# Optimization experiments

Hardware: AMD Instinct MI355X
Metric: run time of the kernel (lower is better)

## Reference

```python
import jax, jax.numpy as jnp
import numpy as np

KH, KW = 3, 3
SH, SW = 1, 1
DH, DW = 1, 1
OFFSET_GROUPS = 1
WEIGHT_GROUPS = 1


def setup_inputs() -> dict:
    key = jax.random.key(0)
    k1, k2, k3, k4 = jax.random.split(key, 4)
    B, C, H, W = 8, 128, 64, 64
    F = 128
    x = jax.random.normal(k1, (B, C, H, W), dtype=jnp.float32)
    offset = jax.random.normal(k2, (B, OFFSET_GROUPS * 2 * KH * KW, H, W), dtype=jnp.float32)
    mask = jax.random.uniform(k3, (B, OFFSET_GROUPS * KH * KW, H, W), dtype=jnp.float32)
    weight = jax.random.normal(k4, (F, C // WEIGHT_GROUPS, KH, KW), dtype=jnp.float32) * 0.05
    return {"x": x, "offset": offset, "mask": mask, "weight": weight}


def _deform_conv2d(x, offset, mask, weight):
    B, C, H, W = x.shape
    F = weight.shape[0]
    Ho, Wo = offset.shape[2], offset.shape[3]
    KK = KH * KW
    og = OFFSET_GROUPS
    Cg = C // og

    # SAME padding (TF convention, symmetric-ish: extra pad at bottom/right)
    pad_h = max((Ho - 1) * SH + (KH - 1) * DH + 1 - H, 0)
    pad_w = max((Wo - 1) * SW + (KW - 1) * DW + 1 - W, 0)
    pad_t, pad_l = pad_h // 2, pad_w // 2

    # offsets laid out as [B, og, KK, (dy,dx), Ho, Wo]
    off = offset.reshape(B, og, KK, 2, Ho, Wo)
    dy, dx = off[:, :, :, 0], off[:, :, :, 1]  # [B, og, KK, Ho, Wo]

    ki, kj = jnp.meshgrid(jnp.arange(KH), jnp.arange(KW), indexing="ij")
    ki = ki.reshape(KK)
    kj = kj.reshape(KK)
    base_y = (jnp.arange(Ho) * SH - pad_t)[None, :] + (ki * DH)[:, None]  # [KK, Ho]
    base_x = (jnp.arange(Wo) * SW - pad_l)[None, :] + (kj * DW)[:, None]  # [KK, Wo]

    py = base_y[None, None, :, :, None].astype(x.dtype) + dy  # [B, og, KK, Ho, Wo]
    px = base_x[None, None, :, None, :].astype(x.dtype) + dx

    y0 = jnp.floor(py)
    x0 = jnp.floor(px)
    ly = py - y0  # fractional parts
    lx = px - x0
    hy = 1.0 - ly
    hx = 1.0 - lx
    y0i = y0.astype(jnp.int32)
    x0i = x0.astype(jnp.int32)

    xg = x.reshape(B, og, Cg, H * W)

    def gather_corner(yi, xi):
        valid = (yi >= 0) & (yi < H) & (xi >= 0) & (xi < W)  # [B, og, KK, Ho, Wo]
        yc = jnp.clip(yi, 0, H - 1)
        xc = jnp.clip(xi, 0, W - 1)
        flat = (yc * W + xc).reshape(B, og, 1, KK * Ho * Wo)
        vals = jnp.take_along_axis(xg, flat, axis=3).reshape(B, og, Cg, KK, Ho, Wo)
        return vals * valid[:, :, None].astype(x.dtype)

    v00 = gather_corner(y0i, x0i)
    v01 = gather_corner(y0i, x0i + 1)
    v10 = gather_corner(y0i + 1, x0i)
    v11 = gather_corner(y0i + 1, x0i + 1)

    w00 = (hy * hx)[:, :, None]
    w01 = (hy * lx)[:, :, None]
    w10 = (ly * hx)[:, :, None]
    w11 = (ly * lx)[:, :, None]
    sampled = v00 * w00 + v01 * w01 + v10 * w10 + v11 * w11  # [B, og, Cg, KK, Ho, Wo]

    # modulation mask: [B, og, KK, Ho, Wo]
    m = mask.reshape(B, og, KK, Ho, Wo)
    sampled = sampled * m[:, :, None]

    # grouped matmul (weight_groups=1 -> plain); columns ordered c*KK + kk, matching
    # weight [F, C, KH, KW] flattened.
    cols = sampled.reshape(B, C * KK, Ho, Wo)
    out = jnp.einsum("fk,bkhw->bfhw", weight.reshape(F, C // WEIGHT_GROUPS * KK), cols)
    return out


def reference(x, offset, mask, weight):
    return _deform_conv2d(x, offset, mask, weight)
```

## Files before the change

kernel.cpp:

```cpp
#include <hip/hip_runtime.h>
#include <hip/hip_bf16.h>

typedef __attribute__((ext_vector_type(8))) short bf16x8;
typedef __attribute__((ext_vector_type(4))) float f32x4;
typedef __attribute__((ext_vector_type(2))) float f32x2;
typedef unsigned int uint32;
typedef unsigned short ushort_t;
typedef __attribute__((ext_vector_type(4))) uint32 u32x4;

__device__ __forceinline__ ushort_t f2bf(float f) {
    unsigned int u = __float_as_uint(f);
    u = (u + 0x7FFFu + ((u >> 16) & 1u)) >> 16;
    return (ushort_t)u;
}

__device__ __forceinline__ uint32 cvt_pk_bf16(float lo, float hi) {
    uint32 r;
    asm("v_cvt_pk_bf16_f32 %0, %1, %2" : "=v"(r) : "v"(lo), "v"(hi));
    return r;
}

__device__ __forceinline__ void gload_lds16(const void* g, void* l) {
    __builtin_amdgcn_global_load_lds(
        (const __attribute__((address_space(1))) uint32*)g,
        (__attribute__((address_space(3))) uint32*)l, 16, 0, 0);
}

__global__ __launch_bounds__(256) void prep_all(const float* __restrict__ x,
                                                const float* __restrict__ w,
                                                ushort_t* __restrict__ xt,
                                                ushort_t* __restrict__ wT2) {
    int bi = blockIdx.x;
    int t = threadIdx.x;
    if (bi >= 4096) {
        int idx = (bi - 4096) * 256 + t;
        int j  = idx & 7;
        int f  = (idx >> 3) & 127;
        int lu = (idx >> 10) & 3;
        int ks = (idx >> 12) & 3;
        int tap = idx >> 14;
        int c = ks * 32 + lu * 8 + j;
        wT2[idx] = f2bf(w[((size_t)f * 128 + c) * 9 + tap]);
        return;
    }
    __shared__ float tile[32][33];
    int b = bi & 7;
    int r2 = bi >> 3;
    int wb = r2 & 1, cb = (r2 >> 1) & 3, y = r2 >> 3;
    int lw = t & 31, lc = t >> 5;
    #pragma unroll
    for (int pass = 0; pass < 4; ++pass) {
        int c = cb * 32 + lc + pass * 8;
        tile[lc + pass * 8][lw] = x[(((size_t)b * 128 + c) * 64 + y) * 64 + wb * 32 + lw];
    }
    __syncthreads();
    int cc = t & 31, xl = t >> 5;
    #pragma unroll
    for (int pass = 0; pass < 4; ++pass) {
        int xll = xl + pass * 8;
        int xx = wb * 32 + xll;
        int c = cb * 32 + cc;
        int c2 = (((c >> 3) ^ (xx & 7)) << 3) | (c & 7);
        xt[(((size_t)b * 64 + y) * 64 + xx) * 128 + c2] = f2bf(tile[cc][xll]);
    }
}

__device__ __forceinline__ bf16x8 interp4(u32x4 c0, u32x4 c1, u32x4 c2, u32x4 c3,
                                          f32x4 wv) {
    uint32 rr[4];
    #pragma unroll
    for (int i = 0; i < 4; ++i) {
        f32x2 a, s;
        uint32 u = c0[i];
        a.x = __uint_as_float(u << 16); a.y = __uint_as_float(u & 0xffff0000u);
        s = a * wv.x;
        u = c1[i];
        a.x = __uint_as_float(u << 16); a.y = __uint_as_float(u & 0xffff0000u);
        s += a * wv.y;
        u = c2[i];
        a.x = __uint_as_float(u << 16); a.y = __uint_as_float(u & 0xffff0000u);
        s += a * wv.z;
        u = c3[i];
        a.x = __uint_as_float(u << 16); a.y = __uint_as_float(u & 0xffff0000u);
        s += a * wv.w;
        rr[i] = cvt_pk_bf16(s.x, s.y);
    }
    u32x4 q = {rr[0], rr[1], rr[2], rr[3]};
    return __builtin_bit_cast(bf16x8, q);
}

__global__ __launch_bounds__(1024, 4) void dcn_main(
    const float* __restrict__ offset, const float* __restrict__ mask,
    const ushort_t* __restrict__ xt, const ushort_t* __restrict__ wT2,
    float* __restrict__ out)
{
    __shared__ ushort_t xwin[7 * 64 * 128];
    __shared__ float  pws_l[9][64][4];
    __shared__ uint32 pos_l[9][64];

    int bi = blockIdx.x;
    int b = bi & 7, ho = bi >> 3;
    int t = threadIdx.x, lane = t & 63, wid = t >> 6;
    int pxg = wid & 3, ks = wid >> 2;
    int p = lane & 15, lu = lane >> 4;
    int px = pxg * 16 + p;
    int row0 = min(max(ho - 3, 0), 57);

    const char* xgb = (const char*)xt + (size_t)b * (64 * 64 * 256);

    {
        const char* ws = xgb + ((size_t)row0 << 14);
        #pragma unroll
        for (int r = 0; r < 7; ++r)
            gload_lds16(ws + (r * 1024 + t) * 16, (char*)xwin + (r * 1024 + t) * 16);
    }
    if (t < 576) {
        int k = t >> 6, pi = t & 63;
        int ki = k / 3, kj = k - ki * 3;
        float dy = offset[(((size_t)b * 18 + 2 * k)     * 64 + ho) * 64 + pi];
        float dx = offset[(((size_t)b * 18 + 2 * k + 1) * 64 + ho) * 64 + pi];
        float m  = mask  [(((size_t)b * 9  + k)         * 64 + ho) * 64 + pi];
        float py = (float)(ho - 1 + ki) + dy;
        float px_ = (float)(pi - 1 + kj) + dx;
        float y0f = floorf(py), x0f = floorf(px_);
        float ly = py - y0f, lx = px_ - x0f;
        float hy = 1.f - ly, hx = 1.f - lx;
        int y0 = (int)y0f, x0 = (int)x0f;
        int y1 = y0 + 1, x1 = x0 + 1;
        float vy0 = (y0 >= 0 && y0 < 64) ? 1.f : 0.f;
        float vy1 = (y1 >= 0 && y1 < 64) ? 1.f : 0.f;
        float vx0 = (x0 >= 0 && x0 < 64) ? 1.f : 0.f;
        float vx1 = (x1 >= 0 && x1 < 64) ? 1.f : 0.f;
        pws_l[k][pi][0] = hy * hx * m * vy0 * vx0;
        pws_l[k][pi][1] = hy * lx * m * vy0 * vx1;
        pws_l[k][pi][2] = ly * hx * m * vy1 * vx0;
        pws_l[k][pi][3] = ly * lx * m * vy1 * vx1;
        int y0c = min(max(y0, 0), 63), y1c = min(max(y1, 0), 63);
        int x0c = min(max(x0, 0), 63), x1c = min(max(x1, 0), 63);
        pos_l[k][pi] = (uint32)(y0c * 64 + x0c) | ((uint32)(y1c * 64 + x1c) << 16);
    }
    __syncthreads();

    f32x4 acc[8];
    #pragma unroll
    for (int i = 0; i < 8; ++i) acc[i] = (f32x4){0.f, 0.f, 0.f, 0.f};

    int klu = ks * 64 + lu * 16;

    #pragma unroll 1
    for (int tap = 0; tap < 9; ++tap) {
        uint32 pp = pos_l[tap][px];
        f32x4 wv = *(const f32x4*)pws_l[tap][px];
        int i00 = pp & 0xffffu, i11 = pp >> 16;
        int y0c = i00 >> 6, x0c = i00 & 63;
        int y1c = i11 >> 6, x1c = i11 & 63;
        u32x4 g[4];
        #pragma unroll
        for (int c = 0; c < 4; ++c) {
            int yc = (c < 2) ? y0c : y1c;
            int xc = (c & 1) ? x1c : x0c;
            int rl = yc - row0;
            int off = klu ^ ((xc & 7) << 4);
            bool inw = (unsigned)rl < 7u;
            const char* lp = (const char*)xwin + (((inw ? rl : 0) * 64 + xc) << 8) + off;
            g[c] = *(const u32x4*)lp;
            if (!inw) {
                const char* gp = xgb + (((size_t)yc * 64 + xc) << 8) + off;
                g[c] = *(const u32x4*)gp;
            }
        }
        bf16x8 bb = interp4(g[0], g[1], g[2], g[3], wv);

        const ushort_t* ab = wT2 + (size_t)(tap * 4 + ks) * 4096 + (lu * 128 + p) * 8;
        #pragma unroll
        for (int ft = 0; ft < 8; ++ft) {
            bf16x8 aa = *(const bf16x8*)(ab + ft * 128);
            acc[ft] = __builtin_amdgcn_mfma_f32_16x16x32_bf16(aa, bb, acc[ft], 0, 0, 0);
        }
    }

    __syncthreads();
    float* red = (float*)xwin;

    #define DUMP(SLOT)                                                          \
        do {                                                                    \
            _Pragma("unroll")                                                   \
            for (int ft = 0; ft < 8; ++ft)                                      \
                _Pragma("unroll")                                               \
                for (int r = 0; r < 4; ++r)                                     \
                    red[(SLOT) * 8192 + (ft * 16 + lu * 4 + r) * 64 + px] =     \
                        acc[ft][r];                                             \
        } while (0)
    #define ADDIN(SLOT)                                                         \
        do {                                                                    \
            _Pragma("unroll")                                                   \
            for (int ft = 0; ft < 8; ++ft)                                      \
                _Pragma("unroll")                                               \
                for (int r = 0; r < 4; ++r)                                     \
                    acc[ft][r] += red[(SLOT) * 8192                             \
                        + (ft * 16 + lu * 4 + r) * 64 + px];                    \
        } while (0)

    if (ks == 1) DUMP(0);
    if (ks == 3) DUMP(1);
    __syncthreads();
    if (ks == 0) ADDIN(0);
    if (ks == 2) ADDIN(1);
    __syncthreads();
    if (ks == 2) DUMP(0);
    __syncthreads();
    if (ks == 0) {
        ADDIN(0);
        float* outb = out + (size_t)b * 128 * 4096 + ho * 64;
        #pragma unroll
        for (int ft = 0; ft < 8; ++ft)
            #pragma unroll
            for (int r = 0; r < 4; ++r) {
                int f = ft * 16 + lu * 4 + r;
                outb[(size_t)f * 4096 + px] = acc[ft][r];
            }
    }
    #undef DUMP
    #undef ADDIN
}

extern "C" void kernel_launch(void* const* d_in, const int* in_sizes, int n_in,
                              void* d_out, int out_size, void* d_ws, size_t ws_size,
                              hipStream_t stream) {
    const float* x      = (const float*)d_in[0];
    const float* offset = (const float*)d_in[1];
    const float* mask   = (const float*)d_in[2];
    const float* weight = (const float*)d_in[3];
    float* out = (float*)d_out;

    ushort_t* xt  = (ushort_t*)d_ws;
    ushort_t* wT2 = xt + (size_t)8 * 64 * 64 * 128;
    if (ws_size < (size_t)(8 * 64 * 64 * 128 + 9 * 16384) * 2) return;

    prep_all<<<4672, 256, 0, stream>>>(x, weight, xt, wT2);
    dcn_main<<<512, 1024, 0, stream>>>(offset, mask, xt, wT2, out);
}
```

Before: 41.83 us.

## Process two output rows per block to reuse weights and the LDS window

Each block now computes two output rows (256 blocks instead of 512). It loads an 8-row input window into LDS and runs two MFMA pixel tiles per weight fragment, so every weight load feeds twice as many MFMAs. Bilinear weights are stored as bf16 and per-corner positions are precomputed with an in-window flag, which lets the LDS budget (about 155KB) hold the larger window. The costs are half as many blocks to fill the GPU, more accumulator registers, and slightly lower precision in the interpolation weights.

```diff
diff --git a/kernel.cpp b/kernel.cpp
--- a/kernel.cpp
+++ b/kernel.cpp
@@ -7,6 +7,7 @@
 typedef unsigned int uint32;
 typedef unsigned short ushort_t;
 typedef __attribute__((ext_vector_type(4))) uint32 u32x4;
+typedef __attribute__((ext_vector_type(2))) uint32 u32x2;
 
 __device__ __forceinline__ ushort_t f2bf(float f) {
     unsigned int u = __float_as_uint(f);
@@ -94,34 +95,37 @@
     const ushort_t* __restrict__ xt, const ushort_t* __restrict__ wT2,
     float* __restrict__ out)
 {
-    __shared__ ushort_t xwin[7 * 64 * 128];
-    __shared__ float  pws_l[9][64][4];
-    __shared__ uint32 pos_l[9][64];
+    __shared__ __align__(16) char smem[158720];
+    ushort_t* xwin = (ushort_t*)smem;
+    ushort_t* pwsl = (ushort_t*)(smem + 131072);
+    uint32*   posl = (uint32*)(smem + 140288);
 
     int bi = blockIdx.x;
-    int b = bi & 7, ho = bi >> 3;
+    int b = bi & 7, rp = bi >> 3;
+    int ho0 = rp * 2;
+    int row0 = min(max(ho0 - 3, 0), 56);
     int t = threadIdx.x, lane = t & 63, wid = t >> 6;
-    int pxg = wid & 3, ks = wid >> 2;
+    int ks = wid >> 2, rowg = (wid >> 1) & 1, pxg = wid & 1;
     int p = lane & 15, lu = lane >> 4;
-    int px = pxg * 16 + p;
-    int row0 = min(max(ho - 3, 0), 57);
+    int klu = (ks * 4 + lu) << 4;
 
     const char* xgb = (const char*)xt + (size_t)b * (64 * 64 * 256);
 
     {
         const char* ws = xgb + ((size_t)row0 << 14);
         #pragma unroll
-        for (int r = 0; r < 7; ++r)
+        for (int r = 0; r < 8; ++r)
             gload_lds16(ws + (r * 1024 + t) * 16, (char*)xwin + (r * 1024 + t) * 16);
     }
-    if (t < 576) {
-        int k = t >> 6, pi = t & 63;
+    for (int item = t; item < 1152; item += 1024) {
+        int k = item >> 7, pxx = item & 127;
+        int row = ho0 + (pxx >> 6), wo = pxx & 63;
         int ki = k / 3, kj = k - ki * 3;
-        float dy = offset[(((size_t)b * 18 + 2 * k)     * 64 + ho) * 64 + pi];
-        float dx = offset[(((size_t)b * 18 + 2 * k + 1) * 64 + ho) * 64 + pi];
-        float m  = mask  [(((size_t)b * 9  + k)         * 64 + ho) * 64 + pi];
-        float py = (float)(ho - 1 + ki) + dy;
-        float px_ = (float)(pi - 1 + kj) + dx;
+        float dy = offset[(((size_t)b * 18 + 2 * k)     * 64 + row) * 64 + wo];
+        float dx = offset[(((size_t)b * 18 + 2 * k + 1) * 64 + row) * 64 + wo];
+        float m  = mask  [(((size_t)b * 9  + k)         * 64 + row) * 64 + wo];
+        float py = (float)(row - 1 + ki) + dy;
+        float px_ = (float)(wo - 1 + kj) + dx;
         float y0f = floorf(py), x0f = floorf(px_);
         float ly = py - y0f, lx = px_ - x0f;
         float hy = 1.f - ly, hx = 1.f - lx;
@@ -131,74 +135,100 @@
         float vy1 = (y1 >= 0 && y1 < 64) ? 1.f : 0.f;
         float vx0 = (x0 >= 0 && x0 < 64) ? 1.f : 0.f;
         float vx1 = (x1 >= 0 && x1 < 64) ? 1.f : 0.f;
-        pws_l[k][pi][0] = hy * hx * m * vy0 * vx0;
-        pws_l[k][pi][1] = hy * lx * m * vy0 * vx1;
-        pws_l[k][pi][2] = ly * hx * m * vy1 * vx0;
-        pws_l[k][pi][3] = ly * lx * m * vy1 * vx1;
+        int base = (k * 128 + pxx) * 4;
+        pwsl[base + 0] = f2bf(hy * hx * m * vy0 * vx0);
+        pwsl[base + 1] = f2bf(hy * lx * m * vy0 * vx1);
+        pwsl[base + 2] = f2bf(ly * hx * m * vy1 * vx0);
+        pwsl[base + 3] = f2bf(ly * lx * m * vy1 * vx1);
         int y0c = min(max(y0, 0), 63), y1c = min(max(y1, 0), 63);
         int x0c = min(max(x0, 0), 63), x1c = min(max(x1, 0), 63);
-        pos_l[k][pi] = (uint32)(y0c * 64 + x0c) | ((uint32)(y1c * 64 + x1c) << 16);
-    }
-    __syncthreads();
-
-    f32x4 acc[8];
-    #pragma unroll
-    for (int i = 0; i < 8; ++i) acc[i] = (f32x4){0.f, 0.f, 0.f, 0.f};
-
-    int klu = ks * 64 + lu * 16;
-
-    #pragma unroll 1
-    for (int tap = 0; tap < 9; ++tap) {
-        uint32 pp = pos_l[tap][px];
-        f32x4 wv = *(const f32x4*)pws_l[tap][px];
-        int i00 = pp & 0xffffu, i11 = pp >> 16;
-        int y0c = i00 >> 6, x0c = i00 & 63;
-        int y1c = i11 >> 6, x1c = i11 & 63;
-        u32x4 g[4];
         #pragma unroll
         for (int c = 0; c < 4; ++c) {
             int yc = (c < 2) ? y0c : y1c;
             int xc = (c & 1) ? x1c : x0c;
-            int rl = yc - row0;
-            int off = klu ^ ((xc & 7) << 4);
-            bool inw = (unsigned)rl < 7u;
-            const char* lp = (const char*)xwin + (((inw ? rl : 0) * 64 + xc) << 8) + off;
-            g[c] = *(const u32x4*)lp;
-            if (!inw) {
-                const char* gp = xgb + (((size_t)yc * 64 + xc) << 8) + off;
-                g[c] = *(const u32x4*)gp;
+            uint32 inw = ((unsigned)(yc - row0) < 8u) ? 0x80u : 0u;
+            posl[base + c] = ((uint32)(yc * 64 + xc) << 8) | (uint32)(xc & 7) | inw;
+        }
+    }
+    __syncthreads();
+
+    f32x4 acc[8][2];
+    #pragma unroll
+    for (int i = 0; i < 8; ++i) {
+        acc[i][0] = (f32x4){0.f, 0.f, 0.f, 0.f};
+        acc[i][1] = (f32x4){0.f, 0.f, 0.f, 0.f};
+    }
+
+    int rbase = row0 << 14;
+
+    #pragma unroll 1
+    for (int tap = 0; tap < 9; ++tap) {
+        bf16x8 bfr[2];
+        #pragma unroll
+        for (int tile = 0; tile < 2; ++tile) {
+            int pxi = rowg * 64 + pxg * 32 + tile * 16 + p;
+            int pb = (tap * 128 + pxi) * 4;
+            u32x2 pw = *(const u32x2*)&pwsl[pb];
+            f32x4 wv;
+            wv.x = __uint_as_float(pw.x << 16);
+            wv.y = __uint_as_float(pw.x & 0xffff0000u);
+            wv.z = __uint_as_float(pw.y << 16);
+            wv.w = __uint_as_float(pw.y & 0xffff0000u);
+            u32x4 pv = *(const u32x4*)&posl[pb];
+            u32x4 g[4];
+            #pragma unroll
+            for (int c = 0; c < 4; ++c) {
+                uint32 v = pv[c];
+                int off = klu ^ (((int)v & 7) << 4);
+                int grec = (int)(v & 0xFFFFFF00u);
+                bool inw = (v & 0x80u) != 0;
+                const char* lp = (const char*)xwin + (inw ? (grec - rbase + off) : off);
+                g[c] = *(const u32x4*)lp;
+                if (!inw) {
+                    g[c] = *(const u32x4*)(xgb + grec + off);
+                }
+            }
+            bfr[tile] = interp4(g[0], g[1], g[2], g[3], wv);
+        }
+
+        const ushort_t* ab = wT2 + (size_t)(tap * 4 + ks) * 4096 + (lu * 128 + p) * 8;
+        #pragma unroll
+        for (int fq = 0; fq < 2; ++fq) {
+            #pragma unroll
+            for (int i = 0; i < 4; ++i) {
+                int ft = fq * 4 + i;
+                bf16x8 aa = *(const bf16x8*)(ab + ft * 128);
+                acc[ft][0] = __builtin_amdgcn_mfma_f32_16x16x32_bf16(aa, bfr[0], acc[ft][0], 0, 0, 0);
+                acc[ft][1] = __builtin_amdgcn_mfma_f32_16x16x32_bf16(aa, bfr[1], acc[ft][1], 0, 0, 0);
             }
         }
-        bf16x8 bb = interp4(g[0], g[1], g[2], g[3], wv);
-
-        const ushort_t* ab = wT2 + (size_t)(tap * 4 + ks) * 4096 + (lu * 128 + p) * 8;
-        #pragma unroll
-        for (int ft = 0; ft < 8; ++ft) {
-            bf16x8 aa = *(const bf16x8*)(ab + ft * 128);
-            acc[ft] = __builtin_amdgcn_mfma_f32_16x16x32_bf16(aa, bb, acc[ft], 0, 0, 0);
-        }
-    }
-
-    __syncthreads();
-    float* red = (float*)xwin;
-
-    #define DUMP(SLOT)                                                          \
-        do {                                                                    \
-            _Pragma("unroll")                                                   \
-            for (int ft = 0; ft < 8; ++ft)                                      \
-                _Pragma("unroll")                                               \
-                for (int r = 0; r < 4; ++r)                                     \
-                    red[(SLOT) * 8192 + (ft * 16 + lu * 4 + r) * 64 + px] =     \
-                        acc[ft][r];                                             \
+    }
+
+    __syncthreads();
+    float* red = (float*)smem;
+    int region = rowg * 2 + pxg;
+
+    #define DUMP(SLOT)                                                           \
+        do {                                                                     \
+            _Pragma("unroll")                                                    \
+            for (int ft = 0; ft < 8; ++ft)                                       \
+                _Pragma("unroll")                                                \
+                for (int tile = 0; tile < 2; ++tile)                             \
+                    _Pragma("unroll")                                            \
+                    for (int r = 0; r < 4; ++r)                                  \
+                        red[((((SLOT) * 4 + region) * 128 + ft * 16 + lu * 4 + r)\
+                             * 32) + tile * 16 + p] = acc[ft][tile][r];          \
         } while (0)
-    #define ADDIN(SLOT)                                                         \
-        do {                                                                    \
-            _Pragma("unroll")                                                   \
-            for (int ft = 0; ft < 8; ++ft)                                      \
-                _Pragma("unroll")                                               \
-                for (int r = 0; r < 4; ++r)                                     \
-                    acc[ft][r] += red[(SLOT) * 8192                             \
-                        + (ft * 16 + lu * 4 + r) * 64 + px];                    \
+    #define ADDIN(SLOT)                                                          \
+        do {                                                                     \
+            _Pragma("unroll")                                                    \
+            for (int ft = 0; ft < 8; ++ft)                                       \
+                _Pragma("unroll")                                                \
+                for (int tile = 0; tile < 2; ++tile)                             \
+                    _Pragma("unroll")                                            \
+                    for (int r = 0; r < 4; ++r)                                  \
+                        acc[ft][tile][r] += red[((((SLOT) * 4 + region) * 128    \
+                            + ft * 16 + lu * 4 + r) * 32) + tile * 16 + p];      \
         } while (0)
 
     if (ks == 1) DUMP(0);
@@ -211,14 +241,16 @@
     __syncthreads();
     if (ks == 0) {
         ADDIN(0);
-        float* outb = out + (size_t)b * 128 * 4096 + ho * 64;
+        float* outb = out + (size_t)b * 128 * 4096 + (ho0 + rowg) * 64 + pxg * 32;
         #pragma unroll
         for (int ft = 0; ft < 8; ++ft)
             #pragma unroll
-            for (int r = 0; r < 4; ++r) {
-                int f = ft * 16 + lu * 4 + r;
-                outb[(size_t)f * 4096 + px] = acc[ft][r];
-            }
+            for (int tile = 0; tile < 2; ++tile)
+                #pragma unroll
+                for (int r = 0; r < 4; ++r) {
+                    int f = ft * 16 + lu * 4 + r;
+                    outb[(size_t)f * 4096 + tile * 16 + p] = acc[ft][tile][r];
+                }
     }
     #undef DUMP
     #undef ADDIN
@@ -238,5 +270,5 @@
     if (ws_size < (size_t)(8 * 64 * 64 * 128 + 9 * 16384) * 2) return;
 
     prep_all<<<4672, 256, 0, stream>>>(x, weight, xt, wT2);
-    dcn_main<<<512, 1024, 0, stream>>>(offset, mask, xt, wT2, out);
-}
+    dcn_main<<<256, 1024, 0, stream>>>(offset, mask, xt, wT2, out);
+}
```

After: 48.35 us. 1.16x slower.

## Split channel halves across blocks with atomic output accumulation and taller LDS window

Applied to the files above, without the earlier changes.

Each output row is now handled by two 512-thread blocks, each covering half of the input channels. Each block loads only its 128-byte channel half into a 9-row LDS window, which is taller than the previous 7-row one. The two halves are combined with atomicAdd into an output buffer that the prep kernel now zero-fills. Interpolation weights are stored as bf16, and the global fallback loads are issued after all LDS loads. The change targets occupancy and the cost of the multi-stage LDS reduction, but it adds an output zeroing pass, float atomics with nondeterministic summation order, and reduced weight precision.

```diff
diff --git a/kernel.cpp b/kernel.cpp
--- a/kernel.cpp
+++ b/kernel.cpp
@@ -7,6 +7,8 @@
 typedef unsigned int uint32;
 typedef unsigned short ushort_t;
 typedef __attribute__((ext_vector_type(4))) uint32 u32x4;
+typedef __attribute__((ext_vector_type(2))) uint32 u32x2;
+typedef __attribute__((ext_vector_type(4))) float float4_t;
 
 __device__ __forceinline__ ushort_t f2bf(float f) {
     unsigned int u = __float_as_uint(f);
@@ -29,9 +31,17 @@
 __global__ __launch_bounds__(256) void prep_all(const float* __restrict__ x,
                                                 const float* __restrict__ w,
                                                 ushort_t* __restrict__ xt,
-                                                ushort_t* __restrict__ wT2) {
+                                                ushort_t* __restrict__ wT2,
+                                                float* __restrict__ out) {
     int bi = blockIdx.x;
     int t = threadIdx.x;
+    if (bi >= 4672) {
+        size_t idx = (size_t)(bi - 4672) * 256 + t;
+        float4_t z = (float4_t){0.f, 0.f, 0.f, 0.f};
+        float4_t* o = (float4_t*)out + idx * 4;
+        o[0] = z; o[1] = z; o[2] = z; o[3] = z;
+        return;
+    }
     if (bi >= 4096) {
         int idx = (bi - 4096) * 256 + t;
         int j  = idx & 7;
@@ -60,7 +70,8 @@
         int xll = xl + pass * 8;
         int xx = wb * 32 + xll;
         int c = cb * 32 + cc;
-        int c2 = (((c >> 3) ^ (xx & 7)) << 3) | (c & 7);
+        int sub = (c >> 3) & 7;
+        int c2 = (c & 64) | (((sub ^ (xx & 7)) & 7) << 3) | (c & 7);
         xt[(((size_t)b * 64 + y) * 64 + xx) * 128 + c2] = f2bf(tile[cc][xll]);
     }
 }
@@ -89,33 +100,39 @@
     return __builtin_bit_cast(bf16x8, q);
 }
 
-__global__ __launch_bounds__(1024, 4) void dcn_main(
+__global__ __launch_bounds__(512, 4) void dcn_main(
     const float* __restrict__ offset, const float* __restrict__ mask,
     const ushort_t* __restrict__ xt, const ushort_t* __restrict__ wT2,
     float* __restrict__ out)
 {
-    __shared__ ushort_t xwin[7 * 64 * 128];
-    __shared__ float  pws_l[9][64][4];
-    __shared__ uint32 pos_l[9][64];
+    __shared__ __align__(16) char smem[80640];
+    ushort_t* xwin = (ushort_t*)smem;
+    ushort_t* pwsl = (ushort_t*)(smem + 73728);
+    uint32*   posl = (uint32*)(smem + 78336);
 
     int bi = blockIdx.x;
-    int b = bi & 7, ho = bi >> 3;
+    int b = bi & 7;
+    int rh = bi >> 3;
+    int ho = rh >> 1, h = rh & 1;
     int t = threadIdx.x, lane = t & 63, wid = t >> 6;
-    int pxg = wid & 3, ks = wid >> 2;
+    int pxg = wid & 3, kq = wid >> 2;
     int p = lane & 15, lu = lane >> 4;
     int px = pxg * 16 + p;
-    int row0 = min(max(ho - 3, 0), 57);
+    int row0 = min(max(ho - 4, 0), 55);
+    int ks = h * 2 + kq;
 
     const char* xgb = (const char*)xt + (size_t)b * (64 * 64 * 256);
 
     {
-        const char* ws = xgb + ((size_t)row0 << 14);
-        #pragma unroll
-        for (int r = 0; r < 7; ++r)
-            gload_lds16(ws + (r * 1024 + t) * 16, (char*)xwin + (r * 1024 + t) * 16);
-    }
-    if (t < 576) {
-        int k = t >> 6, pi = t & 63;
+        const char* ws = xgb + ((size_t)row0 << 14) + h * 128;
+        #pragma unroll
+        for (int r = 0; r < 9; ++r) {
+            int i = (r * 512 + t) * 16;
+            gload_lds16(ws + ((size_t)(i >> 7) << 8) + (i & 127), (char*)xwin + i);
+        }
+    }
+    for (int item = t; item < 576; item += 512) {
+        int k = item >> 6, pi = item & 63;
         int ki = k / 3, kj = k - ki * 3;
         float dy = offset[(((size_t)b * 18 + 2 * k)     * 64 + ho) * 64 + pi];
         float dx = offset[(((size_t)b * 18 + 2 * k + 1) * 64 + ho) * 64 + pi];
@@ -131,13 +148,14 @@
         float vy1 = (y1 >= 0 && y1 < 64) ? 1.f : 0.f;
         float vx0 = (x0 >= 0 && x0 < 64) ? 1.f : 0.f;
         float vx1 = (x1 >= 0 && x1 < 64) ? 1.f : 0.f;
-        pws_l[k][pi][0] = hy * hx * m * vy0 * vx0;
-        pws_l[k][pi][1] = hy * lx * m * vy0 * vx1;
-        pws_l[k][pi][2] = ly * hx * m * vy1 * vx0;
-        pws_l[k][pi][3] = ly * lx * m * vy1 * vx1;
+        int base = (k * 64 + pi) * 4;
+        pwsl[base + 0] = f2bf(hy * hx * m * vy0 * vx0);
+        pwsl[base + 1] = f2bf(hy * lx * m * vy0 * vx1);
+        pwsl[base + 2] = f2bf(ly * hx * m * vy1 * vx0);
+        pwsl[base + 3] = f2bf(ly * lx * m * vy1 * vx1);
         int y0c = min(max(y0, 0), 63), y1c = min(max(y1, 0), 63);
         int x0c = min(max(x0, 0), 63), x1c = min(max(x1, 0), 63);
-        pos_l[k][pi] = (uint32)(y0c * 64 + x0c) | ((uint32)(y1c * 64 + x1c) << 16);
+        posl[k * 64 + pi] = (uint32)(y0c * 64 + x0c) | ((uint32)(y1c * 64 + x1c) << 16);
     }
     __syncthreads();
 
@@ -145,33 +163,45 @@
     #pragma unroll
     for (int i = 0; i < 8; ++i) acc[i] = (f32x4){0.f, 0.f, 0.f, 0.f};
 
-    int klu = ks * 64 + lu * 16;
+    int sub = kq * 4 + lu;
+    const ushort_t* abase = wT2 + (lu * 128 + p) * 8;
 
     #pragma unroll 1
     for (int tap = 0; tap < 9; ++tap) {
-        uint32 pp = pos_l[tap][px];
-        f32x4 wv = *(const f32x4*)pws_l[tap][px];
+        uint32 pp = posl[tap * 64 + px];
+        u32x2 pw = *(const u32x2*)&pwsl[(tap * 64 + px) * 4];
+        f32x4 wv;
+        wv.x = __uint_as_float(pw.x << 16);
+        wv.y = __uint_as_float(pw.x & 0xffff0000u);
+        wv.z = __uint_as_float(pw.y << 16);
+        wv.w = __uint_as_float(pw.y & 0xffff0000u);
         int i00 = pp & 0xffffu, i11 = pp >> 16;
         int y0c = i00 >> 6, x0c = i00 & 63;
         int y1c = i11 >> 6, x1c = i11 & 63;
+
         u32x4 g[4];
+        uint32 rec[4];
         #pragma unroll
         for (int c = 0; c < 4; ++c) {
             int yc = (c < 2) ? y0c : y1c;
             int xc = (c & 1) ? x1c : x0c;
             int rl = yc - row0;
-            int off = klu ^ ((xc & 7) << 4);
-            bool inw = (unsigned)rl < 7u;
-            const char* lp = (const char*)xwin + (((inw ? rl : 0) * 64 + xc) << 8) + off;
+            int woff = ((sub ^ (xc & 7)) & 7) << 4;
+            bool inw = (unsigned)rl < 9u;
+            rec[c] = (uint32)(((yc * 64 + xc) << 8) + h * 128 + woff)
+                     | (inw ? 0x80000000u : 0u);
+            const char* lp = (const char*)xwin + (((inw ? rl : 0) * 64 + xc) << 7) + woff;
             g[c] = *(const u32x4*)lp;
-            if (!inw) {
-                const char* gp = xgb + (((size_t)yc * 64 + xc) << 8) + off;
-                g[c] = *(const u32x4*)gp;
-            }
-        }
+        }
+        #pragma unroll
+        for (int c = 0; c < 4; ++c) {
+            if (!(rec[c] & 0x80000000u))
+                g[c] = *(const u32x4*)(xgb + (rec[c] & 0x7fffffffu));
+        }
+
         bf16x8 bb = interp4(g[0], g[1], g[2], g[3], wv);
 
-        const ushort_t* ab = wT2 + (size_t)(tap * 4 + ks) * 4096 + (lu * 128 + p) * 8;
+        const ushort_t* ab = abase + (size_t)(tap * 4 + ks) * 4096;
         #pragma unroll
         for (int ft = 0; ft < 8; ++ft) {
             bf16x8 aa = *(const bf16x8*)(ab + ft * 128);
@@ -180,48 +210,25 @@
     }
 
     __syncthreads();
-    float* red = (float*)xwin;
-
-    #define DUMP(SLOT)                                                          \
-        do {                                                                    \
-            _Pragma("unroll")                                                   \
-            for (int ft = 0; ft < 8; ++ft)                                      \
-                _Pragma("unroll")                                               \
-                for (int r = 0; r < 4; ++r)                                     \
-                    red[(SLOT) * 8192 + (ft * 16 + lu * 4 + r) * 64 + px] =     \
-                        acc[ft][r];                                             \
-        } while (0)
-    #define ADDIN(SLOT)                                                         \
-        do {                                                                    \
-            _Pragma("unroll")                                                   \
-            for (int ft = 0; ft < 8; ++ft)                                      \
-                _Pragma("unroll")                                               \
-                for (int r = 0; r < 4; ++r)                                     \
-                    acc[ft][r] += red[(SLOT) * 8192                             \
-                        + (ft * 16 + lu * 4 + r) * 64 + px];                    \
-        } while (0)
-
-    if (ks == 1) DUMP(0);
-    if (ks == 3) DUMP(1);
-    __syncthreads();
-    if (ks == 0) ADDIN(0);
-    if (ks == 2) ADDIN(1);
-    __syncthreads();
-    if (ks == 2) DUMP(0);
-    __syncthreads();
-    if (ks == 0) {
-        ADDIN(0);
+    float* red = (float*)smem;
+    if (kq == 1) {
+        #pragma unroll
+        for (int ft = 0; ft < 8; ++ft)
+            #pragma unroll
+            for (int r = 0; r < 4; ++r)
+                red[(ft * 16 + lu * 4 + r) * 65 + px] = acc[ft][r];
+    }
+    __syncthreads();
+    if (kq == 0) {
         float* outb = out + (size_t)b * 128 * 4096 + ho * 64;
         #pragma unroll
         for (int ft = 0; ft < 8; ++ft)
             #pragma unroll
             for (int r = 0; r < 4; ++r) {
                 int f = ft * 16 + lu * 4 + r;
-                outb[(size_t)f * 4096 + px] = acc[ft][r];
+                atomicAdd(&outb[(size_t)f * 4096 + px], acc[ft][r] + red[f * 65 + px]);
             }
     }
-    #undef DUMP
-    #undef ADDIN
 }
 
 extern "C" void kernel_launch(void* const* d_in, const int* in_sizes, int n_in,
@@ -237,6 +244,6 @@
     ushort_t* wT2 = xt + (size_t)8 * 64 * 64 * 128;
     if (ws_size < (size_t)(8 * 64 * 64 * 128 + 9 * 16384) * 2) return;
 
-    prep_all<<<4672, 256, 0, stream>>>(x, weight, xt, wT2);
-    dcn_main<<<512, 1024, 0, stream>>>(offset, mask, xt, wT2, out);
-}
+    prep_all<<<5696, 256, 0, stream>>>(x, weight, xt, wT2, out);
+    dcn_main<<<1024, 512, 0, stream>>>(offset, mask, xt, wT2, out);
+}
```

Result: slower. 62.15 us (+48.6%).

## Prefetch weight fragments early, widen LDS window, pad reduction buffer

Applied to the files above, without the earlier changes.

Issues the eight weight-fragment global loads at the top of each tap using inline asm with immediate offsets, and fences them with sched barriers so their latency overlaps the bilinear gather. The out-of-window fallback loads are split into a separate pass. The LDS x-window grows from 7 to 9 rows, so fewer samples fall back to global memory. The reduction scratch gets a row stride of 65 to reduce LDS bank conflicts. In exchange, the larger LDS footprint may lower occupancy, and the explicit vmcnt(0) wait plus asm loads limit what the compiler can schedule.

```diff
diff --git a/kernel.cpp b/kernel.cpp
--- a/kernel.cpp
+++ b/kernel.cpp
@@ -8,6 +8,8 @@
 typedef unsigned short ushort_t;
 typedef __attribute__((ext_vector_type(4))) uint32 u32x4;
 
+#define SB0() __builtin_amdgcn_sched_barrier(0)
+
 __device__ __forceinline__ ushort_t f2bf(float f) {
     unsigned int u = __float_as_uint(f);
     u = (u + 0x7FFFu + ((u >> 16) & 1u)) >> 16;
@@ -17,6 +19,14 @@
 __device__ __forceinline__ uint32 cvt_pk_bf16(float lo, float hi) {
     uint32 r;
     asm("v_cvt_pk_bf16_f32 %0, %1, %2" : "=v"(r) : "v"(lo), "v"(hi));
+    return r;
+}
+
+template<int IMM>
+__device__ __forceinline__ u32x4 gload(const char* p) {
+    u32x4 r;
+    asm volatile("global_load_dwordx4 %0, %1, off offset:%2"
+                 : "=v"(r) : "v"(p), "n"(IMM));
     return r;
 }
 
@@ -94,7 +104,7 @@
     const ushort_t* __restrict__ xt, const ushort_t* __restrict__ wT2,
     float* __restrict__ out)
 {
-    __shared__ ushort_t xwin[7 * 64 * 128];
+    __shared__ ushort_t xwin[9 * 64 * 128];
     __shared__ float  pws_l[9][64][4];
     __shared__ uint32 pos_l[9][64];
 
@@ -104,14 +114,14 @@
     int pxg = wid & 3, ks = wid >> 2;
     int p = lane & 15, lu = lane >> 4;
     int px = pxg * 16 + p;
-    int row0 = min(max(ho - 3, 0), 57);
+    int row0 = min(max(ho - 4, 0), 55);
 
     const char* xgb = (const char*)xt + (size_t)b * (64 * 64 * 256);
 
     {
         const char* ws = xgb + ((size_t)row0 << 14);
         #pragma unroll
-        for (int r = 0; r < 7; ++r)
+        for (int r = 0; r < 9; ++r)
             gload_lds16(ws + (r * 1024 + t) * 16, (char*)xwin + (r * 1024 + t) * 16);
     }
     if (t < 576) {
@@ -146,37 +156,53 @@
     for (int i = 0; i < 8; ++i) acc[i] = (f32x4){0.f, 0.f, 0.f, 0.f};
 
     int klu = ks * 64 + lu * 16;
+    const char* abase = (const char*)wT2 + (lu * 128 + p) * 16;
 
     #pragma unroll 1
     for (int tap = 0; tap < 9; ++tap) {
+        const char* ab = abase + (size_t)(tap * 4 + ks) * 8192;
+        u32x4 a0 = gload<0>(ab),    a1 = gload<256>(ab);
+        u32x4 a2 = gload<512>(ab),  a3 = gload<768>(ab);
+        u32x4 a4 = gload<1024>(ab), a5 = gload<1280>(ab);
+        u32x4 a6 = gload<1536>(ab), a7 = gload<1792>(ab);
+        SB0();
+
         uint32 pp = pos_l[tap][px];
-        f32x4 wv = *(const f32x4*)pws_l[tap][px];
         int i00 = pp & 0xffffu, i11 = pp >> 16;
         int y0c = i00 >> 6, x0c = i00 & 63;
         int y1c = i11 >> 6, x1c = i11 & 63;
         u32x4 g[4];
+        uint32 rec[4];
         #pragma unroll
         for (int c = 0; c < 4; ++c) {
             int yc = (c < 2) ? y0c : y1c;
             int xc = (c & 1) ? x1c : x0c;
             int rl = yc - row0;
             int off = klu ^ ((xc & 7) << 4);
-            bool inw = (unsigned)rl < 7u;
+            bool inw = (unsigned)rl < 9u;
+            rec[c] = (uint32)(((yc * 64 + xc) << 8) + off) | (inw ? 0x80000000u : 0u);
             const char* lp = (const char*)xwin + (((inw ? rl : 0) * 64 + xc) << 8) + off;
             g[c] = *(const u32x4*)lp;
-            if (!inw) {
-                const char* gp = xgb + (((size_t)yc * 64 + xc) << 8) + off;
-                g[c] = *(const u32x4*)gp;
-            }
         }
+        #pragma unroll
+        for (int c = 0; c < 4; ++c) {
+            if (!(rec[c] & 0x80000000u))
+                g[c] = *(const u32x4*)(xgb + (rec[c] & 0x7fffffffu));
+        }
+        f32x4 wv = *(const f32x4*)pws_l[tap][px];
         bf16x8 bb = interp4(g[0], g[1], g[2], g[3], wv);
 
-        const ushort_t* ab = wT2 + (size_t)(tap * 4 + ks) * 4096 + (lu * 128 + p) * 8;
-        #pragma unroll
-        for (int ft = 0; ft < 8; ++ft) {
-            bf16x8 aa = *(const bf16x8*)(ab + ft * 128);
-            acc[ft] = __builtin_amdgcn_mfma_f32_16x16x32_bf16(aa, bb, acc[ft], 0, 0, 0);
-        }
+        asm volatile("s_waitcnt vmcnt(0)" ::: "memory");
+        SB0();
+
+        acc[0] = __builtin_amdgcn_mfma_f32_16x16x32_bf16(__builtin_bit_cast(bf16x8, a0), bb, acc[0], 0, 0, 0);
+        acc[1] = __builtin_amdgcn_mfma_f32_16x16x32_bf16(__builtin_bit_cast(bf16x8, a1), bb, acc[1], 0, 0, 0);
+        acc[2] = __builtin_amdgcn_mfma_f32_16x16x32_bf16(__builtin_bit_cast(bf16x8, a2), bb, acc[2], 0, 0, 0);
+        acc[3] = __builtin_amdgcn_mfma_f32_16x16x32_bf16(__builtin_bit_cast(bf16x8, a3), bb, acc[3], 0, 0, 0);
+        acc[4] = __builtin_amdgcn_mfma_f32_16x16x32_bf16(__builtin_bit_cast(bf16x8, a4), bb, acc[4], 0, 0, 0);
+        acc[5] = __builtin_amdgcn_mfma_f32_16x16x32_bf16(__builtin_bit_cast(bf16x8, a5), bb, acc[5], 0, 0, 0);
+        acc[6] = __builtin_amdgcn_mfma_f32_16x16x32_bf16(__builtin_bit_cast(bf16x8, a6), bb, acc[6], 0, 0, 0);
+        acc[7] = __builtin_amdgcn_mfma_f32_16x16x32_bf16(__builtin_bit_cast(bf16x8, a7), bb, acc[7], 0, 0, 0);
     }
 
     __syncthreads();
@@ -188,7 +214,7 @@
             for (int ft = 0; ft < 8; ++ft)                                      \
                 _Pragma("unroll")                                               \
                 for (int r = 0; r < 4; ++r)                                     \
-                    red[(SLOT) * 8192 + (ft * 16 + lu * 4 + r) * 64 + px] =     \
+                    red[(SLOT) * 8320 + (ft * 16 + lu * 4 + r) * 65 + px] =     \
                         acc[ft][r];                                             \
         } while (0)
     #define ADDIN(SLOT)                                                         \
@@ -197,8 +223,8 @@
             for (int ft = 0; ft < 8; ++ft)                                      \
                 _Pragma("unroll")                                               \
                 for (int r = 0; r < 4; ++r)                                     \
-                    acc[ft][r] += red[(SLOT) * 8192                             \
-                        + (ft * 16 + lu * 4 + r) * 64 + px];                    \
+                    acc[ft][r] += red[(SLOT) * 8320                             \
+                        + (ft * 16 + lu * 4 + r) * 65 + px];                    \
         } while (0)
 
     if (ks == 1) DUMP(0);
```

Measured after the change: 40.99 us (median of 2 runs). -2.0%, faster.
